# Kernel tuning notes

Measured on AMD Instinct MI355X. Metric: run time of the kernel, lower is better.

The kernel has to match this reference:

```python
import jax, jax.numpy as jnp
import numpy as np
from jax import lax

VOCAB = 27
N_EMBD = 512
D_MODEL = 256
PAD_IDX = 26
OUT = 1
B, T = 256, 512


def _lstm_layer(x, w_ih, w_hh, b_ih, b_hh):
    # x: [B, T, in]; w_ih: [4H, in]; w_hh: [4H, H]
    Bb = x.shape[0]
    H = w_hh.shape[1]
    # precompute input contribution to all gates for all timesteps
    xg = jnp.einsum('bti,gi->btg', x, w_ih) + b_ih + b_hh  # [B, T, 4H]

    def step(carry, xg_t):
        h, c = carry
        g = xg_t + h @ w_hh.T  # [B, 4H]
        i, f, gg, o = jnp.split(g, 4, axis=-1)  # PyTorch gate order i,f,g,o
        i = jax.nn.sigmoid(i)
        f = jax.nn.sigmoid(f)
        gg = jnp.tanh(gg)
        o = jax.nn.sigmoid(o)
        c = f * c + i * gg
        h = o * jnp.tanh(c)
        return (h, c), h

    h0 = jnp.zeros((Bb, H), dtype=x.dtype)
    c0 = jnp.zeros((Bb, H), dtype=x.dtype)
    _, ys = lax.scan(step, (h0, c0), jnp.swapaxes(xg, 0, 1))
    return jnp.swapaxes(ys, 0, 1)  # [B, T, H]


def setup_inputs() -> dict:
    key = jax.random.key(0)
    ks = jax.random.split(key, 16)
    s_e = 1.0  # nn.Embedding default init is N(0,1)
    emb = jax.random.normal(ks[0], (VOCAB, N_EMBD), dtype=jnp.float32)
    emb = emb.at[PAD_IDX].set(0.0)
    bound = 1.0 / np.sqrt(D_MODEL)

    def u(k, shape, b):
        return jax.random.uniform(k, shape, dtype=jnp.float32, minval=-b, maxval=b)

    inp = {
        'input_ids': jax.random.randint(ks[1], (B, T), 0, VOCAB, dtype=jnp.int64)
                      if jax.config.jax_enable_x64 else
                      jax.random.randint(ks[1], (B, T), 0, VOCAB).astype(jnp.int32),
        'emb': emb,
        'w_ih0': u(ks[2], (4 * D_MODEL, N_EMBD), bound),
        'w_hh0': u(ks[3], (4 * D_MODEL, D_MODEL), bound),
        'b_ih0': u(ks[4], (4 * D_MODEL,), bound),
        'b_hh0': u(ks[5], (4 * D_MODEL,), bound),
        'w_ih1': u(ks[6], (4 * D_MODEL, D_MODEL), bound),
        'w_hh1': u(ks[7], (4 * D_MODEL, D_MODEL), bound),
        'b_ih1': u(ks[8], (4 * D_MODEL,), bound),
        'b_hh1': u(ks[9], (4 * D_MODEL,), bound),
        'fc1_w': u(ks[10], (D_MODEL // 2, D_MODEL), bound),
        'fc1_b': u(ks[11], (D_MODEL // 2,), bound),
        'fc2_w': u(ks[12], (OUT, D_MODEL // 2), 1.0 / np.sqrt(D_MODEL // 2)),
        'fc2_b': u(ks[13], (OUT,), 1.0 / np.sqrt(D_MODEL // 2)),
    }
    return inp


def reference(input_ids, emb, w_ih0, w_hh0, b_ih0, b_hh0,
              w_ih1, w_hh1, b_ih1, b_hh1, fc1_w, fc1_b, fc2_w, fc2_b):
    # embedding with padding_idx: pad row forced to zero
    table = emb.at[PAD_IDX].set(0.0)
    x = table[input_ids]  # [B, T, n_embd]
    h1 = _lstm_layer(x, w_ih0, w_hh0, b_ih0, b_hh0)   # [B, T, H]
    h2 = _lstm_layer(h1, w_ih1, w_hh1, b_ih1, b_hh1)  # [B, T, H]
    last = h2[:, -1, :]                                # [B, H]
    hidden = jax.nn.relu(last @ fc1_w.T + fc1_b)
    logits = hidden @ fc2_w.T + fc2_b                  # [B, 1]
    return logits
```

## Files before the change

### kernel.cpp

```cpp
#include <hip/hip_runtime.h>

typedef unsigned short u16;
typedef unsigned int u32;
typedef unsigned long long u64;
typedef float f32x2 __attribute__((ext_vector_type(2)));

#define BATCH 256
#define TT 512
#define HID 256
#define GATES 1024
#define NEMB 512
#define VOC 27
#define HPAD 260

__device__ __forceinline__ float bf1(u16 x){ union{u32 u; float f;} v; v.u = ((u32)x) << 16; return v.f; }
__device__ __forceinline__ u16 f2bf(float f){
  union{float f; u32 u;} v; v.f = f;
  u32 u = v.u;
  return (u16)((u + 0x7fffu + ((u >> 16) & 1u)) >> 16);
}
__device__ __forceinline__ float sigm(float x){ return 1.f / (1.f + __expf(-x)); }
__device__ __forceinline__ f32x2 lo2(float4 v){ f32x2 r; r.x = v.x; r.y = v.y; return r; }
__device__ __forceinline__ f32x2 hi2(float4 v){ f32x2 r; r.x = v.z; r.y = v.w; return r; }

__global__ void k_detect(const u16* __restrict__ b, int* __restrict__ flag) {
  int bad = 0;
  for (int k = threadIdx.x; k < 512; k += 64)
    if (((b[2 * k] >> 7) & 0xFF) >= 127) bad = 1;
  unsigned long long m = __ballot(bad);
  if (threadIdx.x == 0) flag[0] = (m != 0ULL) ? 0 : 1;
}

__global__ void k_convert(const void* __restrict__ src, float* __restrict__ dst,
                          int n, const int* __restrict__ flag) {
  int i = blockIdx.x * 256 + threadIdx.x;
  if (i >= n) return;
  dst[i] = flag[0] ? bf1(((const u16*)src)[i]) : ((const float*)src)[i];
}

__global__ void k_prep(const void* __restrict__ emb, const void* __restrict__ wih,
                       const void* __restrict__ bih, const void* __restrict__ bhh,
                       const int* __restrict__ flag, float* __restrict__ W0) {
  int idx = blockIdx.x * 256 + threadIdx.x;
  if (idx >= VOC * GATES) return;
  int v = idx >> 10, g = idx & (GATES - 1);
  int isbf = flag[0];
  float acc = isbf ? (bf1(((const u16*)bih)[g]) + bf1(((const u16*)bhh)[g]))
                   : (((const float*)bih)[g] + ((const float*)bhh)[g]);
  if (v != 26) {
    float s = 0.f;
    if (isbf) {
      const u16* e = (const u16*)emb + v * NEMB;
      const u16* w = (const u16*)wih + g * NEMB;
      for (int i = 0; i < NEMB; i++) s = fmaf(bf1(e[i]), bf1(w[i]), s);
    } else {
      const float* e = (const float*)emb + v * NEMB;
      const float* w = (const float*)wih + g * NEMB;
      for (int i = 0; i < NEMB; i++) s = fmaf(e[i], w[i], s);
    }
    acc += s;
  }
  W0[idx] = acc;
}

__global__ __launch_bounds__(1024) void k_lstm(
    const int* __restrict__ ids, const float* __restrict__ W0,
    const float* __restrict__ whh0, const float* __restrict__ wih1,
    const float* __restrict__ whh1,
    const float* __restrict__ bih1, const float* __restrict__ bhh1,
    float* __restrict__ h0a, float* __restrict__ h0b,
    float* __restrict__ h1a, float* __restrict__ h1b,
    u32* __restrict__ bar)
{
  const int tid = threadIdx.x;
  const int bid = blockIdx.x;
  const int xcd = bid & 7, m = bid >> 3;
  const int bg = xcd * 2 + (m & 1);
  const int jc = m >> 1;

  const int tb = tid & 15;
  const int rr = tid >> 4;
  const int grow = ((rr >> 4) << 8) + (jc << 4) + (rr & 15);

  __shared__ __align__(16) float hp0[2][16][HPAD];
  __shared__ __align__(16) float hp1[16][HPAD];
  __shared__ float gs0[64][17];
  __shared__ float gs1[64][17];
  __shared__ int   ids_l[16][TT + 1];

  const float* wl0 = whh0 + (size_t)grow * HID;
  const float* wi  = wih1 + (size_t)grow * HID;
  const float* wh  = whh1 + (size_t)grow * HID;
  const float bsum = bih1[grow] + bhh1[grow];

  const int pj = tid & 15, pb = (tid >> 4) & 15;
  const int prow = (bg * 16 + pb) * HID + (jc * 16 + pj);
  float c0r = 0.f, c1r = 0.f;

  u32* cnt0 = bar + bg * 64;
  u32* cnt1 = cnt0 + 32;

  #pragma unroll
  for (int u = 0; u < 8; ++u) {
    int e = tid + 1024 * u;
    int b = e >> 9, tt = e & 511;
    ids_l[b][tt] = ids[(bg * 16 + b) * TT + tt];
  }

  for (int t = 0; t <= TT + 1; ++t) {
    if (tid == 0) {
      if (t >= 1 && t <= TT) {
        u32 want = 16u * (u32)t;
        while (__hip_atomic_load(cnt0, __ATOMIC_RELAXED, __HIP_MEMORY_SCOPE_AGENT) < want)
          __builtin_amdgcn_s_sleep(1);
      }
      if (t >= 3) {
        u32 want = 16u * (u32)(t - 2);
        while (__hip_atomic_load(cnt1, __ATOMIC_RELAXED, __HIP_MEMORY_SCOPE_AGENT) < want)
          __builtin_amdgcn_s_sleep(1);
      }
    }
    __syncthreads();

    if (t <= TT) {
      const float* h0p = ((t + 1) & 1) ? h0b : h0a;
      const u64* s0 = (const u64*)(h0p + bg * 16 * HID);
      float (*dst)[HPAD] = hp0[t & 1];
      #pragma unroll
      for (int u = 0; u < 2; ++u) {
        int e = tid + 1024 * u;
        u64 v = __hip_atomic_load(s0 + e, __ATOMIC_RELAXED, __HIP_MEMORY_SCOPE_AGENT);
        *(u64*)&dst[e >> 7][(e & 127) * 2] = v;
      }
    }
    if (t >= 2) {
      const float* h1p = ((t + 1) & 1) ? h1b : h1a;
      const u64* s1 = (const u64*)(h1p + bg * 16 * HID);
      #pragma unroll
      for (int u = 0; u < 2; ++u) {
        int e = tid + 1024 * u;
        u64 v = __hip_atomic_load(s1 + e, __ATOMIC_RELAXED, __HIP_MEMORY_SCOPE_AGENT);
        *(u64*)&hp1[e >> 7][(e & 127) * 2] = v;
      }
    }
    __syncthreads();

    if (t < TT) {
      float xgv = W0[(size_t)ids_l[tb][t] * GATES + grow];
      const float4* w4 = (const float4*)wl0;
      const float4* h4 = (const float4*)hp0[t & 1][tb];
      f32x2 sA = {0.f, 0.f}, sB = {0.f, 0.f};
      #pragma unroll 8
      for (int k = 0; k < 64; ++k) {
        float4 q = w4[k], hv = h4[k];
        sA = lo2(q) * lo2(hv) + sA;
        sB = hi2(q) * hi2(hv) + sB;
      }
      gs0[rr][tb] = xgv + sA.x + sA.y + sB.x + sB.y;
    }
    __syncthreads();

    if (t < TT && tid < 256) {
      float gi = sigm(gs0[pj][pb]);
      float gf = sigm(gs0[16 + pj][pb]);
      float gg = tanhf(gs0[32 + pj][pb]);
      float go = sigm(gs0[48 + pj][pb]);
      c0r = fmaf(gf, c0r, gi * gg);
      float* h0n = (t & 1) ? h0b : h0a;
      __hip_atomic_store(&h0n[prow], go * tanhf(c0r),
                         __ATOMIC_RELAXED, __HIP_MEMORY_SCOPE_AGENT);
    }
    __syncthreads();
    if (tid == 0 && t < TT)
      __hip_atomic_fetch_add(cnt0, 1u, __ATOMIC_RELAXED, __HIP_MEMORY_SCOPE_AGENT);

    if (t >= 2) {
      const float4* wi4 = (const float4*)wi;
      const float4* wh4 = (const float4*)wh;
      const float4* x4  = (const float4*)hp0[(t - 1) & 1][tb];
      const float4* h4  = (const float4*)hp1[tb];
      f32x2 sIa = {0.f,0.f}, sIb = {0.f,0.f}, sHa = {0.f,0.f}, sHb = {0.f,0.f};
      #pragma unroll 8
      for (int k = 0; k < 64; ++k) {
        float4 qi = wi4[k], qh = wh4[k], xv = x4[k], hv = h4[k];
        sIa = lo2(qi) * lo2(xv) + sIa;
        sIb = hi2(qi) * hi2(xv) + sIb;
        sHa = lo2(qh) * lo2(hv) + sHa;
        sHb = hi2(qh) * hi2(hv) + sHb;
      }
      gs1[rr][tb] = bsum + sIa.x + sIa.y + sIb.x + sIb.y
                         + sHa.x + sHa.y + sHb.x + sHb.y;
    }
    __syncthreads();

    if (t >= 2 && tid < 256) {
      float gi = sigm(gs1[pj][pb]);
      float gf = sigm(gs1[16 + pj][pb]);
      float gg = tanhf(gs1[32 + pj][pb]);
      float go = sigm(gs1[48 + pj][pb]);
      c1r = fmaf(gf, c1r, gi * gg);
      float* h1n = (t & 1) ? h1b : h1a;
      __hip_atomic_store(&h1n[prow], go * tanhf(c1r),
                         __ATOMIC_RELAXED, __HIP_MEMORY_SCOPE_AGENT);
    }
    __syncthreads();
    if (tid == 0 && t >= 2 && t <= TT)
      __hip_atomic_fetch_add(cnt1, 1u, __ATOMIC_RELAXED, __HIP_MEMORY_SCOPE_AGENT);
  }
}

__global__ __launch_bounds__(128) void k_fc(
    const float* __restrict__ hfin,
    const void* __restrict__ fc1w, const void* __restrict__ fc1b,
    const void* __restrict__ fc2w, const void* __restrict__ fc2b,
    const int* __restrict__ flag, void* __restrict__ out) {
  int b = blockIdx.x, j = threadIdx.x;
  __shared__ float red[128];
  const float* h = hfin + b * HID;
  int isbf = flag[0];
  float acc = isbf ? bf1(((const u16*)fc1b)[j]) : ((const float*)fc1b)[j];
  if (isbf) {
    const u16* w = (const u16*)fc1w + j * HID;
    for (int k = 0; k < HID; k++) acc = fmaf(bf1(w[k]), h[k], acc);
  } else {
    const float* w = (const float*)fc1w + j * HID;
    for (int k = 0; k < HID; k++) acc = fmaf(w[k], h[k], acc);
  }
  acc = fmaxf(acc, 0.f);
  float w2 = isbf ? bf1(((const u16*)fc2w)[j]) : ((const float*)fc2w)[j];
  red[j] = acc * w2;
  __syncthreads();
  for (int s = 64; s > 0; s >>= 1) {
    if (j < s) red[j] += red[j + s];
    __syncthreads();
  }
  if (j == 0) {
    float b2 = isbf ? bf1(((const u16*)fc2b)[0]) : ((const float*)fc2b)[0];
    float r = red[0] + b2;
    if (isbf) ((u16*)out)[b] = f2bf(r);
    else      ((float*)out)[b] = r;
  }
}

extern "C" void kernel_launch(void* const* d_in, const int* in_sizes, int n_in,
                              void* d_out, int out_size, void* d_ws, size_t ws_size,
                              hipStream_t stream) {
  const int* ids   = (const int*)d_in[0];
  const void* emb  = d_in[1];
  const void* wih0 = d_in[2];
  const void* whh0 = d_in[3];
  const void* bih0 = d_in[4];
  const void* bhh0 = d_in[5];
  const void* wih1 = d_in[6];
  const void* whh1 = d_in[7];
  const void* bih1 = d_in[8];
  const void* bhh1 = d_in[9];
  const void* fc1w = d_in[10];
  const void* fc1b = d_in[11];
  const void* fc2w = d_in[12];
  const void* fc2b = d_in[13];

  float* ws = (float*)d_ws;
  int*   flag    = (int*)ws;
  float* W0emb   = ws + 16;
  float* whh0_f  = W0emb  + VOC * GATES;
  float* wih1_f  = whh0_f + GATES * HID;
  float* whh1_f  = wih1_f + GATES * HID;
  float* bih1_f  = whh1_f + GATES * HID;
  float* bhh1_f  = bih1_f + GATES;
  float* h0A = bhh1_f + GATES;
  float* h0B = h0A + BATCH * HID;
  float* c0  = h0B + BATCH * HID;
  float* h1A = c0  + BATCH * HID;
  float* h1B = h1A + BATCH * HID;
  float* c1  = h1B + BATCH * HID;
  u32*   bar = (u32*)c0;

  k_detect<<<1, 64, 0, stream>>>((const u16*)bih0, flag);

  k_convert<<<(GATES * HID + 255) / 256, 256, 0, stream>>>(whh0, whh0_f, GATES * HID, flag);
  k_convert<<<(GATES * HID + 255) / 256, 256, 0, stream>>>(wih1, wih1_f, GATES * HID, flag);
  k_convert<<<(GATES * HID + 255) / 256, 256, 0, stream>>>(whh1, whh1_f, GATES * HID, flag);
  k_convert<<<(GATES + 255) / 256, 256, 0, stream>>>(bih1, bih1_f, GATES, flag);
  k_convert<<<(GATES + 255) / 256, 256, 0, stream>>>(bhh1, bhh1_f, GATES, flag);

  hipMemsetAsync(h0A, 0, (size_t)6 * BATCH * HID * sizeof(float), stream);

  k_prep<<<(VOC * GATES + 255) / 256, 256, 0, stream>>>(emb, wih0, bih0, bhh0, flag, W0emb);

  k_lstm<<<256, 1024, 0, stream>>>(ids, W0emb, whh0_f, wih1_f, whh1_f,
                                   bih1_f, bhh1_f, h0A, h0B, h1A, h1B, bar);

  k_fc<<<BATCH, 128, 0, stream>>>(h1B, fc1w, fc1b, fc2w, fc2b, flag, d_out);
}
```

Baseline: 13.15 ms.

## Replace atomic counters with per-block flags and split-K gate matvecs

Replaces the shared per-group atomic counter barrier with per-block step flags that one wavefront polls in parallel with a wave-wide all-reduce. Each thread now computes partial dot products for all four gates over a quarter of K and reduces across lanes with shuffles. Both layers' matvecs run in one phase, and the pointwise updates are split onto separate wavefronts, which removes two block barriers per step. The flag protocol relies on an explicit vmcnt wait before each flag store and needs the flag buffer sized for 256*16*2 entries.

```diff
diff --git a/kernel.cpp b/kernel.cpp
--- a/kernel.cpp
+++ b/kernel.cpp
@@ -78,9 +78,11 @@
   const int bg = xcd * 2 + (m & 1);
   const int jc = m >> 1;
 
-  const int tb = tid & 15;
-  const int rr = tid >> 4;
-  const int grow = ((rr >> 4) << 8) + (jc << 4) + (rr & 15);
+  const int tb  = tid & 15;
+  const int ks  = (tid >> 4) & 3;
+  const int j16 = tid >> 6;
+  const int wv  = tid >> 6;
+  const int ln  = tid & 63;
 
   __shared__ __align__(16) float hp0[2][16][HPAD];
   __shared__ __align__(16) float hp1[16][HPAD];
@@ -88,36 +90,45 @@
   __shared__ float gs1[64][17];
   __shared__ int   ids_l[16][TT + 1];
 
-  const float* wl0 = whh0 + (size_t)grow * HID;
-  const float* wi  = wih1 + (size_t)grow * HID;
-  const float* wh  = whh1 + (size_t)grow * HID;
-  const float bsum = bih1[grow] + bhh1[grow];
-
-  const int pj = tid & 15, pb = (tid >> 4) & 15;
-  const int prow = (bg * 16 + pb) * HID + (jc * 16 + pj);
-  float c0r = 0.f, c1r = 0.f;
-
-  u32* cnt0 = bar + bg * 64;
-  u32* cnt1 = cnt0 + 32;
+  int roff[4];
+  #pragma unroll
+  for (int g = 0; g < 4; ++g) roff[g] = (g * 256 + jc * 16 + j16) * HID + ks * 64;
+
+  float bs[4];
+  #pragma unroll
+  for (int g = 0; g < 4; ++g) {
+    int grow = g * 256 + jc * 16 + j16;
+    bs[g] = bih1[grow] + bhh1[grow];
+  }
+
+  float c0r[4] = {0.f, 0.f, 0.f, 0.f};
+  float c1r[4] = {0.f, 0.f, 0.f, 0.f};
+
+  u32* flags0 = bar;
+  u32* flags1 = bar + 256 * 16;
 
   #pragma unroll
   for (int u = 0; u < 8; ++u) {
     int e = tid + 1024 * u;
-    int b = e >> 9, tt = e & 511;
-    ids_l[b][tt] = ids[(bg * 16 + b) * TT + tt];
+    int b = e >> 9, t2 = e & 511;
+    ids_l[b][t2] = ids[(bg * 16 + b) * TT + t2];
   }
 
   for (int t = 0; t <= TT + 1; ++t) {
-    if (tid == 0) {
-      if (t >= 1 && t <= TT) {
-        u32 want = 16u * (u32)t;
-        while (__hip_atomic_load(cnt0, __ATOMIC_RELAXED, __HIP_MEMORY_SCOPE_AGENT) < want)
-          __builtin_amdgcn_s_sleep(1);
-      }
-      if (t >= 3) {
-        u32 want = 16u * (u32)(t - 2);
-        while (__hip_atomic_load(cnt1, __ATOMIC_RELAXED, __HIP_MEMORY_SCOPE_AGENT) < want)
-          __builtin_amdgcn_s_sleep(1);
+    if (wv == 2) {
+      u32 need0 = (t >= 1 && t <= TT) ? (u32)t : 0u;
+      u32 need1 = (t >= 3) ? (u32)(t - 2) : 0u;
+      const u32* fp = nullptr;
+      u32 need = 0;
+      if (ln < 16)      { fp = flags0 + (bg * 16 + ln) * 16;        need = need0; }
+      else if (ln < 32) { fp = flags1 + (bg * 16 + (ln - 16)) * 16; need = need1; }
+      if (need) {
+        for (;;) {
+          bool ok = true;
+          if (fp) ok = __hip_atomic_load(fp, __ATOMIC_RELAXED, __HIP_MEMORY_SCOPE_AGENT) >= need;
+          if (__all(ok)) break;
+          __builtin_amdgcn_s_sleep(2);
+        }
       }
     }
     __syncthreads();
@@ -146,66 +157,128 @@
     __syncthreads();
 
     if (t < TT) {
-      float xgv = W0[(size_t)ids_l[tb][t] * GATES + grow];
-      const float4* w4 = (const float4*)wl0;
-      const float4* h4 = (const float4*)hp0[t & 1][tb];
-      f32x2 sA = {0.f, 0.f}, sB = {0.f, 0.f};
-      #pragma unroll 8
-      for (int k = 0; k < 64; ++k) {
-        float4 q = w4[k], hv = h4[k];
-        sA = lo2(q) * lo2(hv) + sA;
-        sB = hi2(q) * hi2(hv) + sB;
-      }
-      gs0[rr][tb] = xgv + sA.x + sA.y + sB.x + sB.y;
+      float xg0 = 0.f, xg1 = 0.f, xg2 = 0.f, xg3 = 0.f;
+      if ((tid & 48) == 0) {
+        const float* xr = W0 + (size_t)ids_l[tb][t] * GATES + jc * 16 + j16;
+        xg0 = xr[0]; xg1 = xr[256]; xg2 = xr[512]; xg3 = xr[768];
+      }
+      const float4* h4 = (const float4*)&hp0[t & 1][tb][ks * 64];
+      const float4* w0 = (const float4*)(whh0 + roff[0]);
+      const float4* w1 = (const float4*)(whh0 + roff[1]);
+      const float4* w2 = (const float4*)(whh0 + roff[2]);
+      const float4* w3 = (const float4*)(whh0 + roff[3]);
+      f32x2 aL0={0,0}, aH0={0,0}, aL1={0,0}, aH1={0,0};
+      f32x2 aL2={0,0}, aH2={0,0}, aL3={0,0}, aH3={0,0};
+      #pragma unroll 4
+      for (int k = 0; k < 16; ++k) {
+        float4 hv = h4[k];
+        float4 q0 = w0[k], q1 = w1[k], q2 = w2[k], q3 = w3[k];
+        aL0 = lo2(q0) * lo2(hv) + aL0; aH0 = hi2(q0) * hi2(hv) + aH0;
+        aL1 = lo2(q1) * lo2(hv) + aL1; aH1 = hi2(q1) * hi2(hv) + aH1;
+        aL2 = lo2(q2) * lo2(hv) + aL2; aH2 = hi2(q2) * hi2(hv) + aH2;
+        aL3 = lo2(q3) * lo2(hv) + aL3; aH3 = hi2(q3) * hi2(hv) + aH3;
+      }
+      float s0 = aL0.x + aL0.y + aH0.x + aH0.y;
+      float s1 = aL1.x + aL1.y + aH1.x + aH1.y;
+      float s2 = aL2.x + aL2.y + aH2.x + aH2.y;
+      float s3 = aL3.x + aL3.y + aH3.x + aH3.y;
+      s0 += __shfl_xor(s0, 16); s0 += __shfl_xor(s0, 32);
+      s1 += __shfl_xor(s1, 16); s1 += __shfl_xor(s1, 32);
+      s2 += __shfl_xor(s2, 16); s2 += __shfl_xor(s2, 32);
+      s3 += __shfl_xor(s3, 16); s3 += __shfl_xor(s3, 32);
+      if ((tid & 48) == 0) {
+        gs0[ 0 + j16][tb] = s0 + xg0;
+        gs0[16 + j16][tb] = s1 + xg1;
+        gs0[32 + j16][tb] = s2 + xg2;
+        gs0[48 + j16][tb] = s3 + xg3;
+      }
+    }
+
+    if (t >= 2) {
+      const float4* x4 = (const float4*)&hp0[(t - 1) & 1][tb][ks * 64];
+      const float4* h4 = (const float4*)&hp1[tb][ks * 64];
+      const float4* wi0 = (const float4*)(wih1 + roff[0]);
+      const float4* wi1 = (const float4*)(wih1 + roff[1]);
+      const float4* wi2 = (const float4*)(wih1 + roff[2]);
+      const float4* wi3 = (const float4*)(wih1 + roff[3]);
+      const float4* wh0 = (const float4*)(whh1 + roff[0]);
+      const float4* wh1 = (const float4*)(whh1 + roff[1]);
+      const float4* wh2 = (const float4*)(whh1 + roff[2]);
+      const float4* wh3 = (const float4*)(whh1 + roff[3]);
+      f32x2 aL0={0,0}, aH0={0,0}, aL1={0,0}, aH1={0,0};
+      f32x2 aL2={0,0}, aH2={0,0}, aL3={0,0}, aH3={0,0};
+      #pragma unroll 2
+      for (int k = 0; k < 16; ++k) {
+        float4 xv = x4[k], hv = h4[k];
+        float4 qi0 = wi0[k], qi1 = wi1[k], qi2 = wi2[k], qi3 = wi3[k];
+        aL0 = lo2(qi0) * lo2(xv) + aL0; aH0 = hi2(qi0) * hi2(xv) + aH0;
+        aL1 = lo2(qi1) * lo2(xv) + aL1; aH1 = hi2(qi1) * hi2(xv) + aH1;
+        aL2 = lo2(qi2) * lo2(xv) + aL2; aH2 = hi2(qi2) * hi2(xv) + aH2;
+        aL3 = lo2(qi3) * lo2(xv) + aL3; aH3 = hi2(qi3) * hi2(xv) + aH3;
+        float4 qh0 = wh0[k], qh1 = wh1[k], qh2 = wh2[k], qh3 = wh3[k];
+        aL0 = lo2(qh0) * lo2(hv) + aL0; aH0 = hi2(qh0) * hi2(hv) + aH0;
+        aL1 = lo2(qh1) * lo2(hv) + aL1; aH1 = hi2(qh1) * hi2(hv) + aH1;
+        aL2 = lo2(qh2) * lo2(hv) + aL2; aH2 = hi2(qh2) * hi2(hv) + aH2;
+        aL3 = lo2(qh3) * lo2(hv) + aL3; aH3 = hi2(qh3) * hi2(hv) + aH3;
+      }
+      float s0 = aL0.x + aL0.y + aH0.x + aH0.y;
+      float s1 = aL1.x + aL1.y + aH1.x + aH1.y;
+      float s2 = aL2.x + aL2.y + aH2.x + aH2.y;
+      float s3 = aL3.x + aL3.y + aH3.x + aH3.y;
+      s0 += __shfl_xor(s0, 16); s0 += __shfl_xor(s0, 32);
+      s1 += __shfl_xor(s1, 16); s1 += __shfl_xor(s1, 32);
+      s2 += __shfl_xor(s2, 16); s2 += __shfl_xor(s2, 32);
+      s3 += __shfl_xor(s3, 16); s3 += __shfl_xor(s3, 32);
+      if ((tid & 48) == 0) {
+        gs1[ 0 + j16][tb] = s0 + bs[0];
+        gs1[16 + j16][tb] = s1 + bs[1];
+        gs1[32 + j16][tb] = s2 + bs[2];
+        gs1[48 + j16][tb] = s3 + bs[3];
+      }
     }
     __syncthreads();
 
-    if (t < TT && tid < 256) {
-      float gi = sigm(gs0[pj][pb]);
-      float gf = sigm(gs0[16 + pj][pb]);
-      float gg = tanhf(gs0[32 + pj][pb]);
-      float go = sigm(gs0[48 + pj][pb]);
-      c0r = fmaf(gf, c0r, gi * gg);
+    if (wv == 0 && t < TT) {
       float* h0n = (t & 1) ? h0b : h0a;
-      __hip_atomic_store(&h0n[prow], go * tanhf(c0r),
-                         __ATOMIC_RELAXED, __HIP_MEMORY_SCOPE_AGENT);
-    }
-    __syncthreads();
-    if (tid == 0 && t < TT)
-      __hip_atomic_fetch_add(cnt0, 1u, __ATOMIC_RELAXED, __HIP_MEMORY_SCOPE_AGENT);
-
-    if (t >= 2) {
-      const float4* wi4 = (const float4*)wi;
-      const float4* wh4 = (const float4*)wh;
-      const float4* x4  = (const float4*)hp0[(t - 1) & 1][tb];
-      const float4* h4  = (const float4*)hp1[tb];
-      f32x2 sIa = {0.f,0.f}, sIb = {0.f,0.f}, sHa = {0.f,0.f}, sHb = {0.f,0.f};
-      #pragma unroll 8
-      for (int k = 0; k < 64; ++k) {
-        float4 qi = wi4[k], qh = wh4[k], xv = x4[k], hv = h4[k];
-        sIa = lo2(qi) * lo2(xv) + sIa;
-        sIb = hi2(qi) * hi2(xv) + sIb;
-        sHa = lo2(qh) * lo2(hv) + sHa;
-        sHb = hi2(qh) * hi2(hv) + sHb;
-      }
-      gs1[rr][tb] = bsum + sIa.x + sIa.y + sIb.x + sIb.y
-                         + sHa.x + sHa.y + sHb.x + sHb.y;
-    }
-    __syncthreads();
-
-    if (t >= 2 && tid < 256) {
-      float gi = sigm(gs1[pj][pb]);
-      float gf = sigm(gs1[16 + pj][pb]);
-      float gg = tanhf(gs1[32 + pj][pb]);
-      float go = sigm(gs1[48 + pj][pb]);
-      c1r = fmaf(gf, c1r, gi * gg);
+      #pragma unroll
+      for (int u = 0; u < 4; ++u) {
+        int c = ln + 64 * u;
+        int pb = c >> 4, pj = c & 15;
+        float gi = sigm(gs0[pj][pb]);
+        float gf = sigm(gs0[16 + pj][pb]);
+        float gg = tanhf(gs0[32 + pj][pb]);
+        float go = sigm(gs0[48 + pj][pb]);
+        c0r[u] = fmaf(gf, c0r[u], gi * gg);
+        __hip_atomic_store(&h0n[(bg * 16 + pb) * HID + jc * 16 + pj],
+                           go * tanhf(c0r[u]),
+                           __ATOMIC_RELAXED, __HIP_MEMORY_SCOPE_AGENT);
+      }
+      asm volatile("s_waitcnt vmcnt(0)" ::: "memory");
+      if (ln == 0)
+        __hip_atomic_store(&flags0[(bg * 16 + jc) * 16], (u32)(t + 1),
+                           __ATOMIC_RELAXED, __HIP_MEMORY_SCOPE_AGENT);
+    }
+
+    if (wv == 1 && t >= 2) {
       float* h1n = (t & 1) ? h1b : h1a;
-      __hip_atomic_store(&h1n[prow], go * tanhf(c1r),
-                         __ATOMIC_RELAXED, __HIP_MEMORY_SCOPE_AGENT);
-    }
-    __syncthreads();
-    if (tid == 0 && t >= 2 && t <= TT)
-      __hip_atomic_fetch_add(cnt1, 1u, __ATOMIC_RELAXED, __HIP_MEMORY_SCOPE_AGENT);
+      #pragma unroll
+      for (int u = 0; u < 4; ++u) {
+        int c = ln + 64 * u;
+        int pb = c >> 4, pj = c & 15;
+        float gi = sigm(gs1[pj][pb]);
+        float gf = sigm(gs1[16 + pj][pb]);
+        float gg = tanhf(gs1[32 + pj][pb]);
+        float go = sigm(gs1[48 + pj][pb]);
+        c1r[u] = fmaf(gf, c1r[u], gi * gg);
+        __hip_atomic_store(&h1n[(bg * 16 + pb) * HID + jc * 16 + pj],
+                           go * tanhf(c1r[u]),
+                           __ATOMIC_RELAXED, __HIP_MEMORY_SCOPE_AGENT);
+      }
+      asm volatile("s_waitcnt vmcnt(0)" ::: "memory");
+      if (ln == 0)
+        __hip_atomic_store(&flags1[(bg * 16 + jc) * 16], (u32)(t - 1),
+                           __ATOMIC_RELAXED, __HIP_MEMORY_SCOPE_AGENT);
+    }
   }
 }
 
```

New measurement: 16.59 ms. 1.26x slower.
